# Performance work log

Hardware: AMD Instinct MI355X
Metric: run time of the kernel (lower is better)

The kernel has to match this reference:

```python
import jax, jax.numpy as jnp
import numpy as np

LEAK = 0.1
K = 16  # nsample

def leaky(x):
    return jnp.where(x > 0, x, LEAK * x)

def setup_inputs() -> dict:
    key = jax.random.key(0)
    ks = jax.random.split(key, 16)
    B, N, C, D = 2, 8192, 128, 128
    s = 0.05
    return {
        "xyz1": jax.random.normal(ks[0], (B, 3, N), jnp.float32),
        "xyz2": jax.random.normal(ks[1], (B, 3, N), jnp.float32),
        "points1": jax.random.normal(ks[2], (B, C, N), jnp.float32),
        "points2": jax.random.normal(ks[3], (B, C, N), jnp.float32),
        "W_t11": jax.random.normal(ks[4], (D, C), jnp.float32) * s,
        "b_t11": jax.random.normal(ks[5], (D,), jnp.float32) * s,
        "W_t22": jax.random.normal(ks[6], (D, C), jnp.float32) * s,
        "b_t22": jax.random.normal(ks[7], (D,), jnp.float32) * s,
        "W_pos": jax.random.normal(ks[8], (D, 3), jnp.float32) * s,
        "b_pos": jax.random.normal(ks[9], (D,), jnp.float32) * s,
        "W_mlp1": jax.random.normal(ks[10], (D, D), jnp.float32) * s,
        "b_mlp1": jax.random.normal(ks[11], (D,), jnp.float32) * s,
        "W_mlp2": jax.random.normal(ks[12], (D, D), jnp.float32) * s,
        "b_mlp2": jax.random.normal(ks[13], (D,), jnp.float32) * s,
    }

def reference(xyz1, xyz2, points1, points2,
              W_t11, b_t11, W_t22, b_t22, W_pos, b_pos,
              W_mlp1, b_mlp1, W_mlp2, b_mlp2):
    # xyz*: [B,3,N], points*: [B,C,N]
    x1 = jnp.transpose(xyz1, (0, 2, 1))  # [B,N1,3]
    x2 = jnp.transpose(xyz2, (0, 2, 1))  # [B,N2,3]
    # 1x1 conv1d (t11/t22) -> [B,N,D]
    p1 = jnp.einsum('dc,bcn->bnd', W_t11, points1) + b_t11
    p2 = jnp.einsum('dc,bcn->bnd', W_t22, points2) + b_t22
    # squared distances [B,N1,N2]
    dist = (jnp.sum(x1 ** 2, -1)[:, :, None]
            + jnp.sum(x2 ** 2, -1)[:, None, :]
            - 2.0 * jnp.einsum('bnc,bmc->bnm', x1, x2))
    _, idx = jax.lax.top_k(-dist, K)  # [B,N1,K] nearest neighbors
    gather = jax.vmap(lambda pts, ix: pts[ix])  # per-batch fancy index
    nbr_xyz = gather(x2, idx)   # [B,N1,K,3]
    g2 = gather(p2, idx)        # [B,N1,K,D]
    direction = nbr_xyz - x1[:, :, None, :]
    pos = jnp.einsum('dc,bnkc->bnkd', W_pos, direction) + b_pos
    new_pts = leaky(g2 + p1[:, :, None, :] + pos)  # BN is Identity (use_bn=False)
    new_pts = leaky(jnp.einsum('dc,bnkc->bnkd', W_mlp1, new_pts) + b_mlp1)
    new_pts = leaky(jnp.einsum('dc,bnkc->bnkd', W_mlp2, new_pts) + b_mlp2)
    out = jnp.max(new_pts, axis=2)  # max over nsample -> [B,N1,D]
    return jnp.transpose(out, (0, 2, 1))  # [B,D,N1] like torch
```

## Files before the change

### kernel.cpp

```cpp
#include <hip/hip_runtime.h>
#include <hip/hip_bf16.h>

static constexpr int B_ = 2;
static constexpr int N_ = 8192;
static constexpr int C_ = 128;
static constexpr int D_ = 128;
static constexpr int K_ = 16;

typedef float f32x4 __attribute__((ext_vector_type(4)));
typedef short s16x8 __attribute__((ext_vector_type(8)));

__device__ __forceinline__ float lrelu(float x) { return fmaxf(x, 0.1f * x); }
__device__ __forceinline__ unsigned short f2bf(float f) {
  __hip_bfloat16 h = __float2bfloat16(f);
  unsigned short u;
  __builtin_memcpy(&u, &h, 2);
  return u;
}
__device__ __forceinline__ float bfl(unsigned int u) { return __uint_as_float(u << 16); }
__device__ __forceinline__ float bfh(unsigned int u) { return __uint_as_float(u & 0xffff0000u); }
__device__ __forceinline__ float rfl(float v) {
  return __uint_as_float((unsigned int)__builtin_amdgcn_readfirstlane((int)__float_as_uint(v)));
}
__device__ __forceinline__ unsigned int mflip(unsigned int x) {
  return x ^ (((unsigned int)(((int)x) >> 31)) | 0x80000000u);
}

__global__ __launch_bounds__(256) void prep_kernel(
    const float* __restrict__ Wt11, const float* __restrict__ Wt22,
    const float* __restrict__ Wm1, const float* __restrict__ Wm2,
    const float* __restrict__ Wpos, const float* __restrict__ xyz2,
    const float* __restrict__ bt11, const float* __restrict__ bpos,
    float* __restrict__ Wt1T, float* __restrict__ Wt2T,
    unsigned short* __restrict__ w1bf, unsigned short* __restrict__ w2bf,
    float* __restrict__ wpx, float* __restrict__ wpy, float* __restrict__ wpz,
    float* __restrict__ b1c, f32x4* __restrict__ cand4) {
  int i = blockIdx.x * 256 + threadIdx.x;
  if (i < C_ * D_) {
    int d = i >> 7, c = i & 127;
    Wt1T[c * D_ + d] = Wt11[i];
    Wt2T[c * D_ + d] = Wt22[i];
    w1bf[i] = f2bf(Wm1[i]);
    w2bf[i] = f2bf(Wm2[i]);
    if (i < D_) {
      wpx[i] = Wpos[i * 3 + 0];
      wpy[i] = Wpos[i * 3 + 1];
      wpz[i] = Wpos[i * 3 + 2];
      b1c[i] = bt11[i] + bpos[i];
    }
    int bb = i >> 13, m = i & 8191;
    const float* s2 = xyz2 + (size_t)bb * 3 * N_;
    float x = s2[m], y = s2[N_ + m], z = s2[2 * N_ + m];
    f32x4 c4;
    c4[0] = -x; c4[1] = -y; c4[2] = -z;
    c4[3] = 0.5f * (x * x + y * y + z * z);
    cand4[(size_t)bb * N_ + m] = c4;
  }
}

__device__ __forceinline__ void conv_body(
    char* smem, int cbid,
    const float* __restrict__ pts, const float* __restrict__ WT,
    const float* __restrict__ bias, unsigned short* __restrict__ dst) {
  float (*tile)[32] = (float(*)[32])smem;
  int b = cbid >> 8;
  int n0 = (cbid & 255) << 5;
  int t = threadIdx.x;
  const float* src = pts + (size_t)b * C_ * N_ + n0;
  for (int i = t; i < C_ * 32; i += 256) {
    int c = i >> 5, nl = i & 31;
    tile[c][nl] = src[(size_t)c * N_ + nl];
  }
  __syncthreads();
  int w = t >> 6, lane = t & 63;
  int nl = lane & 31;
  int d0 = w * 32 + (lane >> 5) * 16;
  float acc[16];
#pragma unroll
  for (int j = 0; j < 16; ++j) acc[j] = 0.f;
  for (int c = 0; c < C_; ++c) {
    float x = tile[c][nl];
    const f32x4* wp = (const f32x4*)(WT + c * D_ + d0);
#pragma unroll
    for (int j = 0; j < 4; ++j) {
      f32x4 wv = wp[j];
#pragma unroll
      for (int q = 0; q < 4; ++q) acc[4 * j + q] += wv[q] * x;
    }
  }
  unsigned short* drow = dst + ((size_t)(b * N_ + n0 + nl)) * D_ + d0;
#pragma unroll
  for (int j8 = 0; j8 < 2; ++j8) {
    uint4 ov;
    unsigned int us[8];
#pragma unroll
    for (int e = 0; e < 8; ++e)
      us[e] = f2bf(acc[8 * j8 + e] + bias[d0 + 8 * j8 + e]);
    ov.x = us[0] | (us[1] << 16);
    ov.y = us[2] | (us[3] << 16);
    ov.z = us[4] | (us[5] << 16);
    ov.w = us[6] | (us[7] << 16);
    *(uint4*)(drow + 8 * j8) = ov;
  }
}

__device__ __forceinline__ void knn_body(
    char* smem, int kbid,
    const float* __restrict__ xyz1, const f32x4* __restrict__ cand4,
    int* __restrict__ idx_out) {
  float (*dmsh)[2][8][64] = (float(*)[2][8][64])smem;
  unsigned long long (*keybuf)[128] = (unsigned long long(*)[128])smem;
  unsigned int (*idxbuf)[8][128] = (unsigned int(*)[8][128])(smem + 8192);
  unsigned int (*icnt)[8] = (unsigned int(*)[8])(smem + 16384);

  int b = kbid >> 9;
  int q0 = (kbid & 511) << 4;
  int t = threadIdx.x;
  int w = t >> 6, lane = t & 63;
  int g = w >> 1, h = w & 1;
  int qbase = q0 + (g << 3);

  const float* s1 = xyz1 + (size_t)b * 3 * N_;
  const f32x4* cbf = cand4 + (size_t)b * N_;
  const f32x4* cb = cbf + (h << 12);

  if (t < 16) icnt[t >> 3][t & 7] = 0u;

  float qx[8], qy[8], qz[8], dmin[8];
#pragma unroll
  for (int qq = 0; qq < 8; ++qq) {
    int q = qbase + qq;
    qx[qq] = rfl(s1[q]);
    qy[qq] = rfl(s1[N_ + q]);
    qz[qq] = rfl(s1[2 * N_ + q]);
    dmin[qq] = 1e30f;
  }

  {
    f32x4 p0 = cb[lane], p1 = cb[64 + lane], p2 = cb[128 + lane], p3 = cb[192 + lane];
    auto proc1 = [&](f32x4 c) {
#pragma unroll
      for (int qq = 0; qq < 8; ++qq) {
        float s = __builtin_fmaf(c[0], qx[qq],
                  __builtin_fmaf(c[1], qy[qq],
                  __builtin_fmaf(c[2], qz[qq], c[3])));
        dmin[qq] = fminf(dmin[qq], s);
      }
    };
    for (int i = 0; i < 60; i += 4) {
      f32x4 c0 = p0; p0 = cb[((i + 4) << 6) + lane]; proc1(c0);
      f32x4 c1 = p1; p1 = cb[((i + 5) << 6) + lane]; proc1(c1);
      f32x4 c2 = p2; p2 = cb[((i + 6) << 6) + lane]; proc1(c2);
      f32x4 c3 = p3; p3 = cb[((i + 7) << 6) + lane]; proc1(c3);
    }
    proc1(p0); proc1(p1); proc1(p2); proc1(p3);
  }

#pragma unroll
  for (int qq = 0; qq < 8; ++qq) dmsh[g][h][qq][lane] = dmin[qq];
  __syncthreads();

  float thr[8];
#pragma unroll 1
  for (int qq = 0; qq < 8; ++qq) {
    unsigned int u0 = mflip(__float_as_uint(dmin[qq]));
    unsigned int u1 = mflip(__float_as_uint(dmsh[g][1 ^ h][qq][lane]));
    unsigned int sel = 0;
    for (int bit = 31; bit >= 0; --bit) {
      unsigned int trial = sel | (1u << bit);
      int c_lt = __popcll(__ballot(u0 < trial)) + __popcll(__ballot(u1 < trial));
      sel = (c_lt < 16) ? trial : sel;
    }
    unsigned int su = sel ^ ((sel & 0x80000000u) ? 0x80000000u : 0xFFFFFFFFu);
    float tf = __uint_as_float(su);
    thr[qq] = tf + (1e-4f + 4e-7f * fabsf(tf));
  }

  {
    f32x4 p0 = cb[lane], p1 = cb[64 + lane], p2 = cb[128 + lane], p3 = cb[192 + lane];
    int mo = (h << 12) + lane;
    auto proc2 = [&](f32x4 c, int m) {
#pragma unroll
      for (int qq = 0; qq < 8; ++qq) {
        float s = __builtin_fmaf(c[0], qx[qq],
                  __builtin_fmaf(c[1], qy[qq],
                  __builtin_fmaf(c[2], qz[qq], c[3])));
        if (s <= thr[qq]) {
          unsigned int pos = atomicAdd(&icnt[g][qq], 1u);
          if (pos < 128u) idxbuf[g][qq][pos] = (unsigned int)m;
        }
      }
    };
    for (int i = 0; i < 60; i += 4) {
      f32x4 c0 = p0; p0 = cb[((i + 4) << 6) + lane]; proc2(c0, mo + (i << 6));
      f32x4 c1 = p1; p1 = cb[((i + 5) << 6) + lane]; proc2(c1, mo + ((i + 1) << 6));
      f32x4 c2 = p2; p2 = cb[((i + 6) << 6) + lane]; proc2(c2, mo + ((i + 2) << 6));
      f32x4 c3 = p3; p3 = cb[((i + 7) << 6) + lane]; proc2(c3, mo + ((i + 3) << 6));
    }
    proc2(p0, mo + (60 << 6));
    proc2(p1, mo + (61 << 6));
    proc2(p2, mo + (62 << 6));
    proc2(p3, mo + (63 << 6));
  }
  __syncthreads();

#pragma unroll 1
  for (int j = 0; j < 4; ++j) {
    int wq = (w << 2) + j;
    int g2 = wq >> 3, qq2 = wq & 7;
    int q = q0 + wq;
    float qx2 = rfl(s1[q]);
    float qy2 = rfl(s1[N_ + q]);
    float qz2 = rfl(s1[2 * N_ + q]);
    int Cq = (int)icnt[g2][qq2];
    if (Cq > 128) Cq = 128;
    bool v0 = lane < Cq;
    unsigned int i0v = v0 ? idxbuf[g2][qq2][lane] : 0u;
    f32x4 c0 = cbf[i0v];
    float t0x = c0[0] + qx2, t0y = c0[1] + qy2, t0z = c0[2] + qz2;
    float d0 = __builtin_fmaf(t0x, t0x, __builtin_fmaf(t0y, t0y, t0z * t0z));
    unsigned long long key0 =
        v0 ? ((((unsigned long long)__float_as_uint(d0)) << 13) | i0v) : ~0ull;
    unsigned long long key1 = ~0ull;
    unsigned int i1v = 0;
    if (Cq > 64) {
      bool v1 = (lane + 64) < Cq;
      i1v = v1 ? idxbuf[g2][qq2][lane + 64] : 0u;
      f32x4 c1 = cbf[i1v];
      float t1x = c1[0] + qx2, t1y = c1[1] + qy2, t1z = c1[2] + qz2;
      float d1 = __builtin_fmaf(t1x, t1x, __builtin_fmaf(t1y, t1y, t1z * t1z));
      key1 = v1 ? ((((unsigned long long)__float_as_uint(d1)) << 13) | i1v) : ~0ull;
    }
    keybuf[w][lane] = key0;
    keybuf[w][lane + 64] = key1;
    int rank0 = 0, rank1 = 0;
    for (int j2 = 0; j2 < Cq; ++j2) {
      unsigned long long kj = keybuf[w][j2];
      rank0 += (kj < key0) ? 1 : 0;
      rank1 += (kj < key1) ? 1 : 0;
    }
    int* dst = idx_out + (((size_t)b * N_ + q) << 4);
    if (v0 && rank0 < K_) dst[rank0] = (int)i0v;
    if (key1 != ~0ull && rank1 < K_) dst[rank1] = (int)i1v;
  }
}

__global__ __launch_bounds__(256, 8) void fat_kernel(
    const float* __restrict__ xyz1, const f32x4* __restrict__ cand4,
    int* __restrict__ idx_out,
    const float* __restrict__ points1, const float* __restrict__ points2,
    const float* __restrict__ Wt1T, const float* __restrict__ Wt2T,
    const float* __restrict__ b1c, const float* __restrict__ bt22,
    unsigned short* __restrict__ p1b, unsigned short* __restrict__ p2b) {
  __shared__ __align__(16) char smem[16448];
  int bid = blockIdx.x;
  if (bid < 1024) {
    knn_body(smem, bid, xyz1, cand4, idx_out);
  } else if (bid < 1536) {
    conv_body(smem, bid - 1024, points1, Wt1T, b1c, p1b);
  } else {
    conv_body(smem, bid - 1536, points2, Wt2T, bt22, p2b);
  }
}

__global__ __launch_bounds__(256, 4) void fuse_kernel(
    const float* __restrict__ xyz1, const float* __restrict__ xyz2,
    const unsigned short* __restrict__ p1b, const unsigned short* __restrict__ p2b,
    const int* __restrict__ idxb,
    const unsigned short* __restrict__ w1bf, const unsigned short* __restrict__ w2bf,
    const float* __restrict__ wpx, const float* __restrict__ wpy,
    const float* __restrict__ wpz,
    const float* __restrict__ b1, const float* __restrict__ b2,
    float* __restrict__ out) {
  __shared__ unsigned char Abuf[32768];
  __shared__ float epib[4][8][32];

  int bid = blockIdx.x;
  int b = bid >> 10;
  int n0 = (bid & 1023) << 3;
  int t = threadIdx.x;
  int wv = t >> 6, lane = t & 63;
  int lrow = lane & 15, lk = lane >> 4;

  s16x8 wfr[2][4];
#pragma unroll
  for (int j2 = 0; j2 < 2; ++j2)
#pragma unroll
    for (int ks = 0; ks < 4; ++ks) {
      int row = wv * 32 + j2 * 16 + lrow;
      wfr[j2][ks] = *(const s16x8*)(w1bf + row * D_ + ks * 32 + lk * 8);
    }

  {
    int row = t >> 1, half = t & 1;
    int nl = row >> 4, kn = row & 15;
    int n = n0 + nl;
    int j = idxb[(((size_t)b * N_ + n) << 4) + kn];
    const float* s1 = xyz1 + (size_t)b * 3 * N_;
    const float* s2 = xyz2 + (size_t)b * 3 * N_;
    float dx = s2[j] - s1[n];
    float dy = s2[N_ + j] - s1[N_ + n];
    float dz = s2[2 * N_ + j] - s1[2 * N_ + n];
    const uint4* g2r = (const uint4*)(p2b + ((size_t)(b * N_ + j)) * D_ + half * 64);
    const uint4* p1r = (const uint4*)(p1b + ((size_t)(b * N_ + n)) * D_ + half * 64);
    int rswz = (row & 7) << 4;
#pragma unroll
    for (int it = 0; it < 8; ++it) {
      int dbase = half * 64 + it * 8;
      uint4 gv = g2r[it];
      uint4 pv = p1r[it];
      float g[8] = {bfl(gv.x), bfh(gv.x), bfl(gv.y), bfh(gv.y),
                    bfl(gv.z), bfh(gv.z), bfl(gv.w), bfh(gv.w)};
      float pp[8] = {bfl(pv.x), bfh(pv.x), bfl(pv.y), bfh(pv.y),
                     bfl(pv.z), bfh(pv.z), bfl(pv.w), bfh(pv.w)};
      f32x4 wxa = *(const f32x4*)(wpx + dbase);
      f32x4 wxb = *(const f32x4*)(wpx + dbase + 4);
      f32x4 wya = *(const f32x4*)(wpy + dbase);
      f32x4 wyb = *(const f32x4*)(wpy + dbase + 4);
      f32x4 wza = *(const f32x4*)(wpz + dbase);
      f32x4 wzb = *(const f32x4*)(wpz + dbase + 4);
      unsigned int us[8];
#pragma unroll
      for (int q = 0; q < 8; ++q) {
        float wx = q < 4 ? wxa[q] : wxb[q - 4];
        float wy = q < 4 ? wya[q] : wyb[q - 4];
        float wz = q < 4 ? wza[q] : wzb[q - 4];
        float v = __builtin_fmaf(wx, dx, __builtin_fmaf(wy, dy,
                  __builtin_fmaf(wz, dz, g[q] + pp[q])));
        us[q] = f2bf(lrelu(v));
      }
      uint4 val4;
      val4.x = us[0] | (us[1] << 16);
      val4.y = us[2] | (us[3] << 16);
      val4.z = us[4] | (us[5] << 16);
      val4.w = us[6] | (us[7] << 16);
      int off = (row << 8) + (dbase << 1);
      *(uint4*)(Abuf + (off ^ rswz)) = val4;
    }
  }
  __syncthreads();

  const f32x4 fzero = {0.f, 0.f, 0.f, 0.f};
  f32x4 acc[8][2];
#pragma unroll
  for (int m = 0; m < 8; ++m) { acc[m][0] = fzero; acc[m][1] = fzero; }

#pragma unroll
  for (int ks = 0; ks < 4; ++ks) {
#pragma unroll
    for (int m = 0; m < 8; ++m) {
      int rw = m * 16 + lrow;
      int off = (rw << 8) + (ks << 6) + (lk << 4);
      s16x8 afr = *(const s16x8*)(Abuf + (off ^ ((rw & 7) << 4)));
      acc[m][0] = __builtin_amdgcn_mfma_f32_16x16x32_bf16(afr, wfr[0][ks], acc[m][0], 0, 0, 0);
      acc[m][1] = __builtin_amdgcn_mfma_f32_16x16x32_bf16(afr, wfr[1][ks], acc[m][1], 0, 0, 0);
    }
  }
  __syncthreads();

#pragma unroll
  for (int j2 = 0; j2 < 2; ++j2)
#pragma unroll
    for (int ks = 0; ks < 4; ++ks) {
      int row = wv * 32 + j2 * 16 + lrow;
      wfr[j2][ks] = *(const s16x8*)(w2bf + row * D_ + ks * 32 + lk * 8);
    }

  {
    float bias1[2];
    bias1[0] = b1[wv * 32 + lrow];
    bias1[1] = b1[wv * 32 + 16 + lrow];
#pragma unroll
    for (int m = 0; m < 8; ++m)
#pragma unroll
      for (int j2 = 0; j2 < 2; ++j2)
#pragma unroll
        for (int r = 0; r < 4; ++r) {
          int rw = m * 16 + lk * 4 + r;
          int col = wv * 32 + j2 * 16 + lrow;
          unsigned short hv = f2bf(lrelu(acc[m][j2][r] + bias1[j2]));
          int off = (rw << 8) + (col << 1);
          *(unsigned short*)(Abuf + (off ^ ((rw & 7) << 4))) = hv;
        }
  }
  __syncthreads();

#pragma unroll
  for (int m = 0; m < 8; ++m) { acc[m][0] = fzero; acc[m][1] = fzero; }

#pragma unroll
  for (int ks = 0; ks < 4; ++ks) {
#pragma unroll
    for (int m = 0; m < 8; ++m) {
      int rw = m * 16 + lrow;
      int off = (rw << 8) + (ks << 6) + (lk << 4);
      s16x8 afr = *(const s16x8*)(Abuf + (off ^ ((rw & 7) << 4)));
      acc[m][0] = __builtin_amdgcn_mfma_f32_16x16x32_bf16(afr, wfr[0][ks], acc[m][0], 0, 0, 0);
      acc[m][1] = __builtin_amdgcn_mfma_f32_16x16x32_bf16(afr, wfr[1][ks], acc[m][1], 0, 0, 0);
    }
  }

  float bias2[2];
  bias2[0] = b2[wv * 32 + lrow];
  bias2[1] = b2[wv * 32 + 16 + lrow];
#pragma unroll
  for (int m = 0; m < 8; ++m) {
#pragma unroll
    for (int j2 = 0; j2 < 2; ++j2) {
      float mx = -1e30f;
#pragma unroll
      for (int r = 0; r < 4; ++r) mx = fmaxf(mx, lrelu(acc[m][j2][r] + bias2[j2]));
      mx = fmaxf(mx, __shfl_xor(mx, 16, 64));
      mx = fmaxf(mx, __shfl_xor(mx, 32, 64));
      if (lk == 0) epib[wv][m][j2 * 16 + lrow] = mx;
    }
  }
  {
    int dl = lane >> 1, nh = lane & 1;
    f32x4 o;
#pragma unroll
    for (int i2 = 0; i2 < 4; ++i2) o[i2] = epib[wv][nh * 4 + i2][dl];
    *(f32x4*)(out + ((size_t)(b * D_ + wv * 32 + dl)) * N_ + n0 + nh * 4) = o;
  }
}

extern "C" void kernel_launch(void* const* d_in, const int* in_sizes, int n_in,
                              void* d_out, int out_size, void* d_ws, size_t ws_size,
                              hipStream_t stream) {
  (void)in_sizes; (void)n_in; (void)out_size; (void)ws_size;
  const float* xyz1    = (const float*)d_in[0];
  const float* xyz2    = (const float*)d_in[1];
  const float* points1 = (const float*)d_in[2];
  const float* points2 = (const float*)d_in[3];
  const float* W_t11   = (const float*)d_in[4];
  const float* b_t11   = (const float*)d_in[5];
  const float* W_t22   = (const float*)d_in[6];
  const float* b_t22   = (const float*)d_in[7];
  const float* W_pos   = (const float*)d_in[8];
  const float* b_pos   = (const float*)d_in[9];
  const float* W_mlp1  = (const float*)d_in[10];
  const float* b_mlp1  = (const float*)d_in[11];
  const float* W_mlp2  = (const float*)d_in[12];
  const float* b_mlp2  = (const float*)d_in[13];
  float* out = (float*)d_out;

  char* ws = (char*)d_ws;
  unsigned short* p1b  = (unsigned short*)(ws);
  unsigned short* p2b  = (unsigned short*)(ws + 4194304);
  float* Wt1T          = (float*)(ws + 8388608);
  float* Wt2T          = (float*)(ws + 8454144);
  unsigned short* w1bf = (unsigned short*)(ws + 8519680);
  unsigned short* w2bf = (unsigned short*)(ws + 8552448);
  float* wpx           = (float*)(ws + 8585216);
  float* wpy           = (float*)(ws + 8585728);
  float* wpz           = (float*)(ws + 8586240);
  f32x4* cand4         = (f32x4*)(ws + 8586752);
  int* idxws           = (int*)(ws + 8848896);
  float* b1c           = (float*)(ws + 9897472);

  prep_kernel<<<64, 256, 0, stream>>>(W_t11, W_t22, W_mlp1, W_mlp2, W_pos, xyz2,
                                      b_t11, b_pos,
                                      Wt1T, Wt2T, w1bf, w2bf, wpx, wpy, wpz,
                                      b1c, cand4);
  fat_kernel<<<2048, 256, 0, stream>>>(xyz1, cand4, idxws,
                                       points1, points2, Wt1T, Wt2T,
                                       b1c, b_t22, p1b, p2b);
  fuse_kernel<<<B_ * 1024, 256, 0, stream>>>(xyz1, xyz2, p1b, p2b, idxws,
                                             w1bf, w2bf, wpx, wpy, wpz,
                                             b_mlp1, b_mlp2, out);
}
```

Measured before the change: 156.2 us.

## Compute KNN distance screening with bf16 MFMA and error-bounded threshold

The KNN candidate scoring now runs on bf16 MFMA 16x16x32 instructions instead of per-lane scalar FMAs. Candidate coordinates are pre-packed into MFMA fragments and their norms stored separately. A global max-abs coordinate is computed in prep and used to widen the selection threshold enough to cover bf16 rounding error. Exact fp32 reranking of survivors is kept, with the candidate buffer grown to 192 entries per query. The costs are extra prep work, a memset, more shared memory and lower occupancy (launch bound 6), plus reliance on the error bound to keep recall exact.

```diff
diff --git a/kernel.cpp b/kernel.cpp
--- a/kernel.cpp
+++ b/kernel.cpp
@@ -6,6 +6,7 @@
 static constexpr int C_ = 128;
 static constexpr int D_ = 128;
 static constexpr int K_ = 16;
+static constexpr int CAP = 192;
 
 typedef float f32x4 __attribute__((ext_vector_type(4)));
 typedef short s16x8 __attribute__((ext_vector_type(8)));
@@ -34,7 +35,8 @@
     float* __restrict__ Wt1T, float* __restrict__ Wt2T,
     unsigned short* __restrict__ w1bf, unsigned short* __restrict__ w2bf,
     float* __restrict__ wpx, float* __restrict__ wpy, float* __restrict__ wpz,
-    float* __restrict__ b1c, f32x4* __restrict__ cand4) {
+    float* __restrict__ b1c, f32x4* __restrict__ cand4,
+    s16x8* __restrict__ candA, float* __restrict__ cnorm, int* __restrict__ cmaxp) {
   int i = blockIdx.x * 256 + threadIdx.x;
   if (i < C_ * D_) {
     int d = i >> 7, c = i & 127;
@@ -54,7 +56,27 @@
     f32x4 c4;
     c4[0] = -x; c4[1] = -y; c4[2] = -z;
     c4[3] = 0.5f * (x * x + y * y + z * z);
-    cand4[(size_t)bb * N_ + m] = c4;
+    cand4[i] = c4;
+    cnorm[i] = c4[3];
+    float am = fmaxf(fmaxf(fabsf(x), fabsf(y)), fabsf(z));
+#pragma unroll
+    for (int s = 1; s < 64; s <<= 1) am = fmaxf(am, __shfl_xor(am, s, 64));
+    if ((threadIdx.x & 63) == 0) atomicMax(cmaxp, __float_as_int(am));
+#pragma unroll
+    for (int rep = 0; rep < 4; ++rep) {
+      int idx = i + rep * 16384;
+      int tile = idx >> 6, slot = idx & 63;
+      int bb2 = tile >> 9, mt = tile & 511;
+      s16x8 frag = (s16x8){0, 0, 0, 0, 0, 0, 0, 0};
+      if (slot < 16) {
+        int m2 = mt * 16 + slot;
+        const float* s2b = xyz2 + (size_t)bb2 * 3 * N_;
+        frag[0] = (short)f2bf(-s2b[m2]);
+        frag[1] = (short)f2bf(-s2b[N_ + m2]);
+        frag[2] = (short)f2bf(-s2b[2 * N_ + m2]);
+      }
+      candA[(size_t)tile * 64 + slot] = frag;
+    }
   }
 }
 
@@ -106,156 +128,179 @@
 
 __device__ __forceinline__ void knn_body(
     char* smem, int kbid,
-    const float* __restrict__ xyz1, const f32x4* __restrict__ cand4,
-    int* __restrict__ idx_out) {
-  float (*dmsh)[2][8][64] = (float(*)[2][8][64])smem;
-  unsigned long long (*keybuf)[128] = (unsigned long long(*)[128])smem;
-  unsigned int (*idxbuf)[8][128] = (unsigned int(*)[8][128])(smem + 8192);
-  unsigned int (*icnt)[8] = (unsigned int(*)[8])(smem + 16384);
+    const float* __restrict__ xyz1, const s16x8* __restrict__ candA,
+    const float* __restrict__ cnorm, const f32x4* __restrict__ cand4,
+    const int* __restrict__ cmaxp, int* __restrict__ idx_out) {
+  unsigned int* idxbuf = (unsigned int*)smem;
+  float* dmsh = (float*)(smem + 12288);
+  unsigned long long* keybuf = (unsigned long long*)(smem + 12288);
+  float* thrsh = (float*)(smem + 18432);
+  unsigned int* icnt = (unsigned int*)(smem + 18496);
 
   int b = kbid >> 9;
   int q0 = (kbid & 511) << 4;
   int t = threadIdx.x;
   int w = t >> 6, lane = t & 63;
-  int g = w >> 1, h = w & 1;
-  int qbase = q0 + (g << 3);
+  int grp = lane >> 4, col = lane & 15;
 
   const float* s1 = xyz1 + (size_t)b * 3 * N_;
-  const f32x4* cbf = cand4 + (size_t)b * N_;
-  const f32x4* cb = cbf + (h << 12);
-
-  if (t < 16) icnt[t >> 3][t & 7] = 0u;
-
-  float qx[8], qy[8], qz[8], dmin[8];
-#pragma unroll
-  for (int qq = 0; qq < 8; ++qq) {
-    int q = qbase + qq;
-    qx[qq] = rfl(s1[q]);
-    qy[qq] = rfl(s1[N_ + q]);
-    qz[qq] = rfl(s1[2 * N_ + q]);
-    dmin[qq] = 1e30f;
-  }
+  const s16x8* cA = candA + ((size_t)b * 512 + (size_t)w * 128) * 64;
+  const float* cnb = cnorm + (size_t)b * N_ + w * 2048;
+
+  if (t < 16) icnt[t] = 0u;
+
+  s16x8 qfrag = (s16x8){0, 0, 0, 0, 0, 0, 0, 0};
+  if (lane < 16) {
+    int q = q0 + lane;
+    qfrag[0] = (short)f2bf(s1[q]);
+    qfrag[1] = (short)f2bf(s1[N_ + q]);
+    qfrag[2] = (short)f2bf(s1[2 * N_ + q]);
+  }
+
+  int cno = grp << 2;
+  const f32x4 big = {1e30f, 1e30f, 1e30f, 1e30f};
+  f32x4 dminv = big;
 
   {
-    f32x4 p0 = cb[lane], p1 = cb[64 + lane], p2 = cb[128 + lane], p3 = cb[192 + lane];
-    auto proc1 = [&](f32x4 c) {
-#pragma unroll
-      for (int qq = 0; qq < 8; ++qq) {
-        float s = __builtin_fmaf(c[0], qx[qq],
-                  __builtin_fmaf(c[1], qy[qq],
-                  __builtin_fmaf(c[2], qz[qq], c[3])));
-        dmin[qq] = fminf(dmin[qq], s);
+    auto P1 = [&](s16x8 af, f32x4 cn) {
+      f32x4 acc = __builtin_amdgcn_mfma_f32_16x16x32_bf16(af, qfrag, cn, 0, 0, 0);
+#pragma unroll
+      for (int r = 0; r < 4; ++r) dminv[r] = fminf(dminv[r], acc[r]);
+    };
+    s16x8 a0 = cA[lane], a1 = cA[64 + lane], a2 = cA[128 + lane], a3 = cA[192 + lane];
+    f32x4 n0 = *(const f32x4*)(cnb + 0 * 16 + cno);
+    f32x4 n1 = *(const f32x4*)(cnb + 1 * 16 + cno);
+    f32x4 n2 = *(const f32x4*)(cnb + 2 * 16 + cno);
+    f32x4 n3 = *(const f32x4*)(cnb + 3 * 16 + cno);
+    for (int ct = 0; ct < 124; ct += 4) {
+      s16x8 c0 = a0; f32x4 m0 = n0;
+      a0 = cA[(ct + 4) * 64 + lane]; n0 = *(const f32x4*)(cnb + (ct + 4) * 16 + cno);
+      P1(c0, m0);
+      s16x8 c1 = a1; f32x4 m1 = n1;
+      a1 = cA[(ct + 5) * 64 + lane]; n1 = *(const f32x4*)(cnb + (ct + 5) * 16 + cno);
+      P1(c1, m1);
+      s16x8 c2 = a2; f32x4 m2 = n2;
+      a2 = cA[(ct + 6) * 64 + lane]; n2 = *(const f32x4*)(cnb + (ct + 6) * 16 + cno);
+      P1(c2, m2);
+      s16x8 c3 = a3; f32x4 m3 = n3;
+      a3 = cA[(ct + 7) * 64 + lane]; n3 = *(const f32x4*)(cnb + (ct + 7) * 16 + cno);
+      P1(c3, m3);
+    }
+    P1(a0, n0); P1(a1, n1); P1(a2, n2); P1(a3, n3);
+  }
+  *(f32x4*)(dmsh + col * 64 + w * 16 + cno) = dminv;
+  __syncthreads();
+
+  {
+    float cmax = __int_as_float(*cmaxp);
+    float c1 = cmax * 0.001953125f * 2.1f;
+    for (int j = 0; j < 4; ++j) {
+      int q = 4 * w + j;
+      int qg = q0 + q;
+      float qxv = rfl(s1[qg]), qyv = rfl(s1[N_ + qg]), qzv = rfl(s1[2 * N_ + qg]);
+      unsigned int u = mflip(__float_as_uint(dmsh[q * 64 + lane]));
+      unsigned int sel = 0;
+      for (int bit = 31; bit >= 0; --bit) {
+        unsigned int trial = sel | (1u << bit);
+        int c_lt = __popcll(__ballot(u < trial));
+        sel = (c_lt < 16) ? trial : sel;
       }
-    };
-    for (int i = 0; i < 60; i += 4) {
-      f32x4 c0 = p0; p0 = cb[((i + 4) << 6) + lane]; proc1(c0);
-      f32x4 c1 = p1; p1 = cb[((i + 5) << 6) + lane]; proc1(c1);
-      f32x4 c2 = p2; p2 = cb[((i + 6) << 6) + lane]; proc1(c2);
-      f32x4 c3 = p3; p3 = cb[((i + 7) << 6) + lane]; proc1(c3);
-    }
-    proc1(p0); proc1(p1); proc1(p2); proc1(p3);
-  }
-
-#pragma unroll
-  for (int qq = 0; qq < 8; ++qq) dmsh[g][h][qq][lane] = dmin[qq];
-  __syncthreads();
-
-  float thr[8];
-#pragma unroll 1
-  for (int qq = 0; qq < 8; ++qq) {
-    unsigned int u0 = mflip(__float_as_uint(dmin[qq]));
-    unsigned int u1 = mflip(__float_as_uint(dmsh[g][1 ^ h][qq][lane]));
-    unsigned int sel = 0;
-    for (int bit = 31; bit >= 0; --bit) {
-      unsigned int trial = sel | (1u << bit);
-      int c_lt = __popcll(__ballot(u0 < trial)) + __popcll(__ballot(u1 < trial));
-      sel = (c_lt < 16) ? trial : sel;
-    }
-    unsigned int su = sel ^ ((sel & 0x80000000u) ? 0x80000000u : 0xFFFFFFFFu);
-    float tf = __uint_as_float(su);
-    thr[qq] = tf + (1e-4f + 4e-7f * fabsf(tf));
-  }
+      unsigned int su = sel ^ ((sel & 0x80000000u) ? 0x80000000u : 0xFFFFFFFFu);
+      float thr = __uint_as_float(su) + 1e-4f +
+                  c1 * (fabsf(qxv) + fabsf(qyv) + fabsf(qzv));
+      if (lane == 0) thrsh[q] = thr;
+    }
+  }
+  __syncthreads();
 
   {
-    f32x4 p0 = cb[lane], p1 = cb[64 + lane], p2 = cb[128 + lane], p3 = cb[192 + lane];
-    int mo = (h << 12) + lane;
-    auto proc2 = [&](f32x4 c, int m) {
-#pragma unroll
-      for (int qq = 0; qq < 8; ++qq) {
-        float s = __builtin_fmaf(c[0], qx[qq],
-                  __builtin_fmaf(c[1], qy[qq],
-                  __builtin_fmaf(c[2], qz[qq], c[3])));
-        if (s <= thr[qq]) {
-          unsigned int pos = atomicAdd(&icnt[g][qq], 1u);
-          if (pos < 128u) idxbuf[g][qq][pos] = (unsigned int)m;
+    float thrv = thrsh[col];
+    int cbase = w * 2048 + cno;
+    auto P2 = [&](s16x8 af, f32x4 cn, int ct) {
+      f32x4 acc = __builtin_amdgcn_mfma_f32_16x16x32_bf16(af, qfrag, cn, 0, 0, 0);
+      float mn = fminf(fminf(acc[0], acc[1]), fminf(acc[2], acc[3]));
+      if (mn <= thrv) {
+#pragma unroll
+        for (int r = 0; r < 4; ++r) {
+          if (acc[r] <= thrv) {
+            unsigned int pos = atomicAdd(&icnt[col], 1u);
+            if (pos < (unsigned)CAP)
+              idxbuf[col * CAP + pos] = (unsigned int)(cbase + ct * 16 + r);
+          }
         }
       }
     };
-    for (int i = 0; i < 60; i += 4) {
-      f32x4 c0 = p0; p0 = cb[((i + 4) << 6) + lane]; proc2(c0, mo + (i << 6));
-      f32x4 c1 = p1; p1 = cb[((i + 5) << 6) + lane]; proc2(c1, mo + ((i + 1) << 6));
-      f32x4 c2 = p2; p2 = cb[((i + 6) << 6) + lane]; proc2(c2, mo + ((i + 2) << 6));
-      f32x4 c3 = p3; p3 = cb[((i + 7) << 6) + lane]; proc2(c3, mo + ((i + 3) << 6));
-    }
-    proc2(p0, mo + (60 << 6));
-    proc2(p1, mo + (61 << 6));
-    proc2(p2, mo + (62 << 6));
-    proc2(p3, mo + (63 << 6));
-  }
-  __syncthreads();
-
+    s16x8 a0 = cA[lane], a1 = cA[64 + lane], a2 = cA[128 + lane], a3 = cA[192 + lane];
+    f32x4 n0 = *(const f32x4*)(cnb + 0 * 16 + cno);
+    f32x4 n1 = *(const f32x4*)(cnb + 1 * 16 + cno);
+    f32x4 n2 = *(const f32x4*)(cnb + 2 * 16 + cno);
+    f32x4 n3 = *(const f32x4*)(cnb + 3 * 16 + cno);
+    for (int ct = 0; ct < 124; ct += 4) {
+      s16x8 c0 = a0; f32x4 m0 = n0;
+      a0 = cA[(ct + 4) * 64 + lane]; n0 = *(const f32x4*)(cnb + (ct + 4) * 16 + cno);
+      P2(c0, m0, ct);
+      s16x8 c1 = a1; f32x4 m1 = n1;
+      a1 = cA[(ct + 5) * 64 + lane]; n1 = *(const f32x4*)(cnb + (ct + 5) * 16 + cno);
+      P2(c1, m1, ct + 1);
+      s16x8 c2 = a2; f32x4 m2 = n2;
+      a2 = cA[(ct + 6) * 64 + lane]; n2 = *(const f32x4*)(cnb + (ct + 6) * 16 + cno);
+      P2(c2, m2, ct + 2);
+      s16x8 c3 = a3; f32x4 m3 = n3;
+      a3 = cA[(ct + 7) * 64 + lane]; n3 = *(const f32x4*)(cnb + (ct + 7) * 16 + cno);
+      P2(c3, m3, ct + 3);
+    }
+    P2(a0, n0, 124); P2(a1, n1, 125); P2(a2, n2, 126); P2(a3, n3, 127);
+  }
+  __syncthreads();
+
+  const f32x4* cb4 = cand4 + (size_t)b * N_;
+  unsigned long long* kb = keybuf + w * CAP;
 #pragma unroll 1
   for (int j = 0; j < 4; ++j) {
-    int wq = (w << 2) + j;
-    int g2 = wq >> 3, qq2 = wq & 7;
-    int q = q0 + wq;
-    float qx2 = rfl(s1[q]);
-    float qy2 = rfl(s1[N_ + q]);
-    float qz2 = rfl(s1[2 * N_ + q]);
-    int Cq = (int)icnt[g2][qq2];
-    if (Cq > 128) Cq = 128;
-    bool v0 = lane < Cq;
-    unsigned int i0v = v0 ? idxbuf[g2][qq2][lane] : 0u;
-    f32x4 c0 = cbf[i0v];
-    float t0x = c0[0] + qx2, t0y = c0[1] + qy2, t0z = c0[2] + qz2;
-    float d0 = __builtin_fmaf(t0x, t0x, __builtin_fmaf(t0y, t0y, t0z * t0z));
-    unsigned long long key0 =
-        v0 ? ((((unsigned long long)__float_as_uint(d0)) << 13) | i0v) : ~0ull;
-    unsigned long long key1 = ~0ull;
-    unsigned int i1v = 0;
-    if (Cq > 64) {
-      bool v1 = (lane + 64) < Cq;
-      i1v = v1 ? idxbuf[g2][qq2][lane + 64] : 0u;
-      f32x4 c1 = cbf[i1v];
-      float t1x = c1[0] + qx2, t1y = c1[1] + qy2, t1z = c1[2] + qz2;
-      float d1 = __builtin_fmaf(t1x, t1x, __builtin_fmaf(t1y, t1y, t1z * t1z));
-      key1 = v1 ? ((((unsigned long long)__float_as_uint(d1)) << 13) | i1v) : ~0ull;
-    }
-    keybuf[w][lane] = key0;
-    keybuf[w][lane + 64] = key1;
-    int rank0 = 0, rank1 = 0;
-    for (int j2 = 0; j2 < Cq; ++j2) {
-      unsigned long long kj = keybuf[w][j2];
-      rank0 += (kj < key0) ? 1 : 0;
-      rank1 += (kj < key1) ? 1 : 0;
-    }
-    int* dst = idx_out + (((size_t)b * N_ + q) << 4);
-    if (v0 && rank0 < K_) dst[rank0] = (int)i0v;
-    if (key1 != ~0ull && rank1 < K_) dst[rank1] = (int)i1v;
-  }
-}
-
-__global__ __launch_bounds__(256, 8) void fat_kernel(
-    const float* __restrict__ xyz1, const f32x4* __restrict__ cand4,
-    int* __restrict__ idx_out,
+    int q = 4 * w + j;
+    int qg = q0 + q;
+    float qxv = rfl(s1[qg]), qyv = rfl(s1[N_ + qg]), qzv = rfl(s1[2 * N_ + qg]);
+    int Cq = (int)icnt[q];
+    if (Cq > CAP) Cq = CAP;
+    unsigned long long keys[3];
+    unsigned int idxs[3];
+#pragma unroll
+    for (int s = 0; s < 3; ++s) {
+      int sl = lane + 64 * s;
+      bool v = sl < Cq;
+      unsigned int iv = v ? idxbuf[q * CAP + sl] : 0u;
+      f32x4 c = cb4[iv];
+      float tx = c[0] + qxv, ty = c[1] + qyv, tz = c[2] + qzv;
+      float d = __builtin_fmaf(tx, tx, __builtin_fmaf(ty, ty, tz * tz));
+      keys[s] = v ? ((((unsigned long long)__float_as_uint(d)) << 13) | iv) : ~0ull;
+      idxs[s] = iv;
+      kb[sl] = keys[s];
+    }
+    int rank[3] = {0, 0, 0};
+    for (int jj = 0; jj < Cq; ++jj) {
+      unsigned long long kj = kb[jj];
+#pragma unroll
+      for (int s = 0; s < 3; ++s) rank[s] += (kj < keys[s]) ? 1 : 0;
+    }
+    int* dst = idx_out + (((size_t)b * N_ + qg) << 4);
+#pragma unroll
+    for (int s = 0; s < 3; ++s)
+      if (keys[s] != ~0ull && rank[s] < K_) dst[rank[s]] = (int)idxs[s];
+  }
+}
+
+__global__ __launch_bounds__(256, 6) void fat_kernel(
+    const float* __restrict__ xyz1, const s16x8* __restrict__ candA,
+    const float* __restrict__ cnorm, const f32x4* __restrict__ cand4,
+    const int* __restrict__ cmaxp, int* __restrict__ idx_out,
     const float* __restrict__ points1, const float* __restrict__ points2,
     const float* __restrict__ Wt1T, const float* __restrict__ Wt2T,
     const float* __restrict__ b1c, const float* __restrict__ bt22,
     unsigned short* __restrict__ p1b, unsigned short* __restrict__ p2b) {
-  __shared__ __align__(16) char smem[16448];
+  __shared__ __align__(16) char smem[18560];
   int bid = blockIdx.x;
   if (bid < 1024) {
-    knn_body(smem, bid, xyz1, cand4, idx_out);
+    knn_body(smem, bid, xyz1, candA, cnorm, cand4, cmaxp, idx_out);
   } else if (bid < 1536) {
     conv_body(smem, bid - 1024, points1, Wt1T, b1c, p1b);
   } else {
@@ -457,12 +502,16 @@
   f32x4* cand4         = (f32x4*)(ws + 8586752);
   int* idxws           = (int*)(ws + 8848896);
   float* b1c           = (float*)(ws + 9897472);
-
+  s16x8* candA         = (s16x8*)(ws + 9898496);
+  float* cnorm         = (float*)(ws + 10947072);
+  int* cmaxp           = (int*)(ws + 11012608);
+
+  hipMemsetAsync(cmaxp, 0, 4, stream);
   prep_kernel<<<64, 256, 0, stream>>>(W_t11, W_t22, W_mlp1, W_mlp2, W_pos, xyz2,
                                       b_t11, b_pos,
                                       Wt1T, Wt2T, w1bf, w2bf, wpx, wpy, wpz,
-                                      b1c, cand4);
-  fat_kernel<<<2048, 256, 0, stream>>>(xyz1, cand4, idxws,
+                                      b1c, cand4, candA, cnorm, cmaxp);
+  fat_kernel<<<2048, 256, 0, stream>>>(xyz1, candA, cnorm, cand4, cmaxp, idxws,
                                        points1, points2, Wt1T, Wt2T,
                                        b1c, b_t22, p1b, p2b);
   fuse_kernel<<<B_ * 1024, 256, 0, stream>>>(xyz1, xyz2, p1b, p2b, idxws,
```

Result: slower. 206.0 us (+31.9%).

## Sort points by z to prune KNN search to a slab window

Applied to the files above, without the earlier changes.

Adds a bitonic sort kernel that orders candidate and query points by z. Each KNN block now handles 16 z-sorted queries. It estimates a threshold from a 2048-candidate window around the queries, then scans only candidates whose z lies within the implied radius, found by binary search. The goal is to avoid the full N-candidate brute-force scan, at the cost of an extra 4-block serial sort launch and irregular per-block work.

```diff
diff --git a/kernel.cpp b/kernel.cpp
--- a/kernel.cpp
+++ b/kernel.cpp
@@ -22,8 +22,23 @@
 __device__ __forceinline__ float rfl(float v) {
   return __uint_as_float((unsigned int)__builtin_amdgcn_readfirstlane((int)__float_as_uint(v)));
 }
+__device__ __forceinline__ int rfli(int v) { return __builtin_amdgcn_readfirstlane(v); }
 __device__ __forceinline__ unsigned int mflip(unsigned int x) {
   return x ^ (((unsigned int)(((int)x) >> 31)) | 0x80000000u);
+}
+__device__ __forceinline__ float unflip(unsigned int u) {
+  u = (u & 0x80000000u) ? (u ^ 0x80000000u) : ~u;
+  return __uint_as_float(u);
+}
+__device__ __forceinline__ int lbound(const float* zs, float v) {
+  int lo = 0, hi = N_;
+  while (lo < hi) { int mid = (lo + hi) >> 1; if (zs[mid] < v) lo = mid + 1; else hi = mid; }
+  return lo;
+}
+__device__ __forceinline__ int ubound(const float* zs, float v) {
+  int lo = 0, hi = N_;
+  while (lo < hi) { int mid = (lo + hi) >> 1; if (zs[mid] <= v) lo = mid + 1; else hi = mid; }
+  return lo;
 }
 
 __global__ __launch_bounds__(256) void prep_kernel(
@@ -58,6 +73,50 @@
   }
 }
 
+__global__ __launch_bounds__(1024) void sort_kernel(
+    const float* __restrict__ xyz1, const float* __restrict__ xyz2,
+    const f32x4* __restrict__ cand4,
+    f32x4* __restrict__ cand4s, float* __restrict__ zsort,
+    unsigned int* __restrict__ cidx, unsigned int* __restrict__ qperm) {
+  __shared__ unsigned long long keys[N_];
+  int blk = blockIdx.x;
+  int t = threadIdx.x;
+  bool isq = blk >= 2;
+  int b = isq ? blk - 2 : blk;
+  const float* src = (isq ? xyz1 : xyz2) + (size_t)b * 3 * N_ + 2 * N_;
+  for (int i = t; i < N_; i += 1024)
+    keys[i] = (((unsigned long long)mflip(__float_as_uint(src[i]))) << 32) | (unsigned)i;
+  for (int k = 2; k <= N_; k <<= 1)
+    for (int j = k >> 1; j > 0; j >>= 1) {
+      __syncthreads();
+      for (int i = t; i < N_; i += 1024) {
+        int p = i ^ j;
+        if (p > i) {
+          unsigned long long a = keys[i], c = keys[p];
+          bool up = ((i & k) == 0);
+          if ((a > c) == up) { keys[i] = c; keys[p] = a; }
+        }
+      }
+    }
+  __syncthreads();
+  if (isq) {
+    unsigned int* qp = qperm + (size_t)b * N_;
+    for (int i = t; i < N_; i += 1024) qp[i] = (unsigned)(keys[i] & 8191ull);
+  } else {
+    f32x4* cs = cand4s + (size_t)b * N_;
+    float* zz = zsort + (size_t)b * N_;
+    unsigned int* ci = cidx + (size_t)b * N_;
+    const f32x4* c4 = cand4 + (size_t)b * N_;
+    for (int i = t; i < N_; i += 1024) {
+      unsigned long long kk = keys[i];
+      unsigned idx = (unsigned)(kk & 8191ull);
+      cs[i] = c4[idx];
+      zz[i] = unflip((unsigned)(kk >> 32));
+      ci[i] = idx;
+    }
+  }
+}
+
 __device__ __forceinline__ void conv_body(
     char* smem, int cbid,
     const float* __restrict__ pts, const float* __restrict__ WT,
@@ -107,116 +166,142 @@
 __device__ __forceinline__ void knn_body(
     char* smem, int kbid,
     const float* __restrict__ xyz1, const f32x4* __restrict__ cand4,
+    const f32x4* __restrict__ cand4s, const float* __restrict__ zsort,
+    const unsigned int* __restrict__ cidx, const unsigned int* __restrict__ qperm,
     int* __restrict__ idx_out) {
-  float (*dmsh)[2][8][64] = (float(*)[2][8][64])smem;
+  float (*dmsh)[16][16] = (float(*)[16][16])smem;
   unsigned long long (*keybuf)[128] = (unsigned long long(*)[128])smem;
-  unsigned int (*idxbuf)[8][128] = (unsigned int(*)[8][128])(smem + 8192);
-  unsigned int (*icnt)[8] = (unsigned int(*)[8])(smem + 16384);
+  unsigned int (*idxbuf)[128] = (unsigned int(*)[128])(smem + 4096);
+  float* thrsh = (float*)(smem + 12288);
+  unsigned int* icnt = (unsigned int*)(smem + 12352);
 
   int b = kbid >> 9;
   int q0 = (kbid & 511) << 4;
-  int t = threadIdx.x;
-  int w = t >> 6, lane = t & 63;
-  int g = w >> 1, h = w & 1;
-  int qbase = q0 + (g << 3);
+  int t = threadIdx.x, w = t >> 6, lane = t & 63;
 
   const float* s1 = xyz1 + (size_t)b * 3 * N_;
-  const f32x4* cbf = cand4 + (size_t)b * N_;
-  const f32x4* cb = cbf + (h << 12);
-
-  if (t < 16) icnt[t >> 3][t & 7] = 0u;
-
-  float qx[8], qy[8], qz[8], dmin[8];
-#pragma unroll
-  for (int qq = 0; qq < 8; ++qq) {
-    int q = qbase + qq;
-    qx[qq] = rfl(s1[q]);
-    qy[qq] = rfl(s1[N_ + q]);
-    qz[qq] = rfl(s1[2 * N_ + q]);
-    dmin[qq] = 1e30f;
-  }
-
+  const f32x4* cbs = cand4s + (size_t)b * N_;
+  const float* zs = zsort + (size_t)b * N_;
+  const unsigned int* ci = cidx + (size_t)b * N_;
+  const unsigned int* qp = qperm + (size_t)b * N_;
+  const f32x4* cb4 = cand4 + (size_t)b * N_;
+
+  if (t < 16) icnt[t] = 0u;
+
+  float qx[16], qy[16], qz[16], qn[16];
+#pragma unroll
+  for (int i = 0; i < 16; ++i) {
+    int qi = rfli((int)qp[q0 + i]);
+    qx[i] = rfl(s1[qi]);
+    qy[i] = rfl(s1[N_ + qi]);
+    qz[i] = rfl(s1[2 * N_ + qi]);
+    qn[i] = qx[i] * qx[i] + qy[i] * qy[i] + qz[i] * qz[i];
+  }
+
+  int center = lbound(zs, qz[7]);
+  int lo0 = center - 1024;
+  lo0 = lo0 < 0 ? 0 : (lo0 > N_ - 2048 ? N_ - 2048 : lo0);
+
+  float dmin[16];
+#pragma unroll
+  for (int i = 0; i < 16; ++i) dmin[i] = 1e30f;
   {
-    f32x4 p0 = cb[lane], p1 = cb[64 + lane], p2 = cb[128 + lane], p3 = cb[192 + lane];
-    auto proc1 = [&](f32x4 c) {
-#pragma unroll
-      for (int qq = 0; qq < 8; ++qq) {
-        float s = __builtin_fmaf(c[0], qx[qq],
-                  __builtin_fmaf(c[1], qy[qq],
-                  __builtin_fmaf(c[2], qz[qq], c[3])));
-        dmin[qq] = fminf(dmin[qq], s);
+    int base = lo0 + (w << 9) + lane;
+#pragma unroll 2
+    for (int g = 0; g < 8; ++g) {
+      f32x4 c = cbs[base + (g << 6)];
+#pragma unroll
+      for (int i = 0; i < 16; ++i) {
+        float s = __builtin_fmaf(c[0], qx[i],
+                  __builtin_fmaf(c[1], qy[i],
+                  __builtin_fmaf(c[2], qz[i], c[3])));
+        dmin[i] = fminf(dmin[i], s);
       }
-    };
-    for (int i = 0; i < 60; i += 4) {
-      f32x4 c0 = p0; p0 = cb[((i + 4) << 6) + lane]; proc1(c0);
-      f32x4 c1 = p1; p1 = cb[((i + 5) << 6) + lane]; proc1(c1);
-      f32x4 c2 = p2; p2 = cb[((i + 6) << 6) + lane]; proc1(c2);
-      f32x4 c3 = p3; p3 = cb[((i + 7) << 6) + lane]; proc1(c3);
-    }
-    proc1(p0); proc1(p1); proc1(p2); proc1(p3);
-  }
-
-#pragma unroll
-  for (int qq = 0; qq < 8; ++qq) dmsh[g][h][qq][lane] = dmin[qq];
-  __syncthreads();
-
-  float thr[8];
+    }
+  }
+#pragma unroll
+  for (int i = 0; i < 16; ++i) {
+    dmin[i] = fminf(dmin[i], __shfl_xor(dmin[i], 16, 64));
+    dmin[i] = fminf(dmin[i], __shfl_xor(dmin[i], 32, 64));
+  }
+  if (lane < 16) {
+#pragma unroll
+    for (int i = 0; i < 16; ++i) dmsh[w][i][lane] = dmin[i];
+  }
+  __syncthreads();
+
 #pragma unroll 1
-  for (int qq = 0; qq < 8; ++qq) {
-    unsigned int u0 = mflip(__float_as_uint(dmin[qq]));
-    unsigned int u1 = mflip(__float_as_uint(dmsh[g][1 ^ h][qq][lane]));
+  for (int j = 0; j < 4; ++j) {
+    int q = (w << 2) + j;
+    unsigned int u = mflip(__float_as_uint(dmsh[lane >> 4][q][lane & 15]));
     unsigned int sel = 0;
     for (int bit = 31; bit >= 0; --bit) {
       unsigned int trial = sel | (1u << bit);
-      int c_lt = __popcll(__ballot(u0 < trial)) + __popcll(__ballot(u1 < trial));
+      int c_lt = __popcll(__ballot(u < trial));
       sel = (c_lt < 16) ? trial : sel;
     }
     unsigned int su = sel ^ ((sel & 0x80000000u) ? 0x80000000u : 0xFFFFFFFFu);
     float tf = __uint_as_float(su);
-    thr[qq] = tf + (1e-4f + 4e-7f * fabsf(tf));
-  }
-
-  {
-    f32x4 p0 = cb[lane], p1 = cb[64 + lane], p2 = cb[128 + lane], p3 = cb[192 + lane];
-    int mo = (h << 12) + lane;
-    auto proc2 = [&](f32x4 c, int m) {
-#pragma unroll
-      for (int qq = 0; qq < 8; ++qq) {
-        float s = __builtin_fmaf(c[0], qx[qq],
-                  __builtin_fmaf(c[1], qy[qq],
-                  __builtin_fmaf(c[2], qz[qq], c[3])));
-        if (s <= thr[qq]) {
-          unsigned int pos = atomicAdd(&icnt[g][qq], 1u);
-          if (pos < 128u) idxbuf[g][qq][pos] = (unsigned int)m;
+    if (lane == 0) thrsh[q] = tf + (1e-4f + 4e-7f * fabsf(tf));
+  }
+  __syncthreads();
+
+  float thrv[16], thrmax = -1e30f;
+#pragma unroll
+  for (int i = 0; i < 16; ++i) { thrv[i] = rfl(thrsh[i]); thrmax = fmaxf(thrmax, thrv[i]); }
+
+  float zlo = 1e30f, zhi = -1e30f;
+#pragma unroll
+  for (int i = 0; i < 16; ++i) {
+    float dthr = fmaxf(__builtin_fmaf(2.0f, thrv[i], qn[i]), 0.0f);
+    float halfw = __builtin_sqrtf(dthr) * 1.0001f + 1e-6f;
+    zlo = fminf(zlo, qz[i] - halfw);
+    zhi = fmaxf(zhi, qz[i] + halfw);
+  }
+  int L = lbound(zs, zlo);
+  int R = ubound(zs, zhi);
+  int nG = (R - L + 63) >> 6;
+
+#pragma unroll 1
+  for (int g = w; g < nG; g += 4) {
+    int rank = L + (g << 6) + lane;
+    bool valid = rank < R;
+    f32x4 c = cbs[valid ? rank : (N_ - 1)];
+    if (!valid) c[3] = 1e30f;
+    float s[16];
+#pragma unroll
+    for (int i = 0; i < 16; ++i)
+      s[i] = __builtin_fmaf(c[0], qx[i],
+             __builtin_fmaf(c[1], qy[i],
+             __builtin_fmaf(c[2], qz[i], c[3])));
+    float mn = s[0];
+#pragma unroll
+    for (int i = 1; i < 16; ++i) mn = fminf(mn, s[i]);
+    if (__any(mn <= thrmax)) {
+      unsigned oi = ci[valid ? rank : 0];
+#pragma unroll
+      for (int i = 0; i < 16; ++i) {
+        if (s[i] <= thrv[i]) {
+          unsigned pos = atomicAdd(&icnt[i], 1u);
+          if (pos < 128u) idxbuf[i][pos] = oi;
         }
       }
-    };
-    for (int i = 0; i < 60; i += 4) {
-      f32x4 c0 = p0; p0 = cb[((i + 4) << 6) + lane]; proc2(c0, mo + (i << 6));
-      f32x4 c1 = p1; p1 = cb[((i + 5) << 6) + lane]; proc2(c1, mo + ((i + 1) << 6));
-      f32x4 c2 = p2; p2 = cb[((i + 6) << 6) + lane]; proc2(c2, mo + ((i + 2) << 6));
-      f32x4 c3 = p3; p3 = cb[((i + 7) << 6) + lane]; proc2(c3, mo + ((i + 3) << 6));
-    }
-    proc2(p0, mo + (60 << 6));
-    proc2(p1, mo + (61 << 6));
-    proc2(p2, mo + (62 << 6));
-    proc2(p3, mo + (63 << 6));
+    }
   }
   __syncthreads();
 
 #pragma unroll 1
   for (int j = 0; j < 4; ++j) {
-    int wq = (w << 2) + j;
-    int g2 = wq >> 3, qq2 = wq & 7;
-    int q = q0 + wq;
-    float qx2 = rfl(s1[q]);
-    float qy2 = rfl(s1[N_ + q]);
-    float qz2 = rfl(s1[2 * N_ + q]);
-    int Cq = (int)icnt[g2][qq2];
+    int q = (w << 2) + j;
+    int qg = rfli((int)qp[q0 + q]);
+    float qx2 = rfl(s1[qg]);
+    float qy2 = rfl(s1[N_ + qg]);
+    float qz2 = rfl(s1[2 * N_ + qg]);
+    int Cq = (int)icnt[q];
     if (Cq > 128) Cq = 128;
     bool v0 = lane < Cq;
-    unsigned int i0v = v0 ? idxbuf[g2][qq2][lane] : 0u;
-    f32x4 c0 = cbf[i0v];
+    unsigned int i0v = v0 ? idxbuf[q][lane] : 0u;
+    f32x4 c0 = cb4[i0v];
     float t0x = c0[0] + qx2, t0y = c0[1] + qy2, t0z = c0[2] + qz2;
     float d0 = __builtin_fmaf(t0x, t0x, __builtin_fmaf(t0y, t0y, t0z * t0z));
     unsigned long long key0 =
@@ -225,8 +310,8 @@
     unsigned int i1v = 0;
     if (Cq > 64) {
       bool v1 = (lane + 64) < Cq;
-      i1v = v1 ? idxbuf[g2][qq2][lane + 64] : 0u;
-      f32x4 c1 = cbf[i1v];
+      i1v = v1 ? idxbuf[q][lane + 64] : 0u;
+      f32x4 c1 = cb4[i1v];
       float t1x = c1[0] + qx2, t1y = c1[1] + qy2, t1z = c1[2] + qz2;
       float d1 = __builtin_fmaf(t1x, t1x, __builtin_fmaf(t1y, t1y, t1z * t1z));
       key1 = v1 ? ((((unsigned long long)__float_as_uint(d1)) << 13) | i1v) : ~0ull;
@@ -239,7 +324,7 @@
       rank0 += (kj < key0) ? 1 : 0;
       rank1 += (kj < key1) ? 1 : 0;
     }
-    int* dst = idx_out + (((size_t)b * N_ + q) << 4);
+    int* dst = idx_out + (((size_t)b * N_ + qg) << 4);
     if (v0 && rank0 < K_) dst[rank0] = (int)i0v;
     if (key1 != ~0ull && rank1 < K_) dst[rank1] = (int)i1v;
   }
@@ -247,15 +332,17 @@
 
 __global__ __launch_bounds__(256, 8) void fat_kernel(
     const float* __restrict__ xyz1, const f32x4* __restrict__ cand4,
+    const f32x4* __restrict__ cand4s, const float* __restrict__ zsort,
+    const unsigned int* __restrict__ cidx, const unsigned int* __restrict__ qperm,
     int* __restrict__ idx_out,
     const float* __restrict__ points1, const float* __restrict__ points2,
     const float* __restrict__ Wt1T, const float* __restrict__ Wt2T,
     const float* __restrict__ b1c, const float* __restrict__ bt22,
     unsigned short* __restrict__ p1b, unsigned short* __restrict__ p2b) {
-  __shared__ __align__(16) char smem[16448];
+  __shared__ __align__(16) char smem[16384];
   int bid = blockIdx.x;
   if (bid < 1024) {
-    knn_body(smem, bid, xyz1, cand4, idx_out);
+    knn_body(smem, bid, xyz1, cand4, cand4s, zsort, cidx, qperm, idx_out);
   } else if (bid < 1536) {
     conv_body(smem, bid - 1024, points1, Wt1T, b1c, p1b);
   } else {
@@ -457,12 +544,17 @@
   f32x4* cand4         = (f32x4*)(ws + 8586752);
   int* idxws           = (int*)(ws + 8848896);
   float* b1c           = (float*)(ws + 9897472);
+  f32x4* cand4s        = (f32x4*)(ws + 9897984);
+  float* zsort         = (float*)(ws + 10160128);
+  unsigned int* cidx   = (unsigned int*)(ws + 10225664);
+  unsigned int* qperm  = (unsigned int*)(ws + 10291200);
 
   prep_kernel<<<64, 256, 0, stream>>>(W_t11, W_t22, W_mlp1, W_mlp2, W_pos, xyz2,
                                       b_t11, b_pos,
                                       Wt1T, Wt2T, w1bf, w2bf, wpx, wpy, wpz,
                                       b1c, cand4);
-  fat_kernel<<<2048, 256, 0, stream>>>(xyz1, cand4, idxws,
+  sort_kernel<<<4, 1024, 0, stream>>>(xyz1, xyz2, cand4, cand4s, zsort, cidx, qperm);
+  fat_kernel<<<2048, 256, 0, stream>>>(xyz1, cand4, cand4s, zsort, cidx, qperm, idxws,
                                        points1, points2, Wt1T, Wt2T,
                                        b1c, b_t22, p1b, p2b);
   fuse_kernel<<<B_ * 1024, 256, 0, stream>>>(xyz1, xyz2, p1b, p2b, idxws,
```

New measurement: 268.7 us. +72.0%, slower.
